# Kernel tuning notes

Hardware: AMD Instinct MI355X
Metric: run time of the kernel (lower is better)

The kernel has to match this reference:

```python
import jax, jax.numpy as jnp
import numpy as np

EDGE_THRESHOLD = 5  # from init_kwargs


def setup_inputs() -> dict:
    key = jax.random.key(0)
    batch = jax.random.normal(key, (2, 512, 192, 256), dtype=jnp.float32)
    return {"batch": batch}


def reference(batch):
    # batch: [b, c, h, w]
    # 1) depth-wise (channel) max
    depth_wise_max = jnp.max(batch, axis=1, keepdims=True)      # [b,1,h,w]
    is_depth_wise_max = batch == depth_wise_max

    # 2) 3x3 local max (stride 1, pad 1) == max_pool2d(3,1,1)
    local_max = jax.lax.reduce_window(
        batch, -jnp.inf, jax.lax.max,
        window_dimensions=(1, 1, 3, 3),
        window_strides=(1, 1, 1, 1),
        padding='SAME')
    is_local_max = batch == local_max

    # 3) fixed 3x3 Hessian stencils via zero-padded shifts (same math as conv2d w/ padding=1)
    z = jnp.pad(batch, ((0, 0), (0, 0), (1, 1), (1, 1)))        # zero pad
    up    = z[:, :, :-2, 1:-1]
    down  = z[:, :, 2:,  1:-1]
    left  = z[:, :, 1:-1, :-2]
    right = z[:, :, 1:-1, 2:]
    dii = up + down - 2.0 * batch                                # [[0,1,0],[0,-2,0],[0,1,0]]
    djj = left + right - 2.0 * batch                             # [[0,0,0],[1,-2,1],[0,0,0]]
    dij = 0.25 * (z[:, :, :-2, :-2] - z[:, :, :-2, 2:]
                  - z[:, :, 2:, :-2] + z[:, :, 2:, 2:])          # 0.25*[[1,0,-1],[0,0,0],[-1,0,1]]

    det = dii * djj - dij * dij
    tr = dii + djj
    threshold = (EDGE_THRESHOLD + 1) ** 2 / EDGE_THRESHOLD
    # torch.min on bool tensors == logical and
    is_not_edge = (tr * tr / det <= threshold) & (det > 0)

    detected = is_depth_wise_max & is_local_max & is_not_edge
    return detected
```

## Files before the change

kernel.cpp:

```cpp
#include <hip/hip_runtime.h>
#include <cstdint>
#include <cstddef>


namespace {

constexpr int Bn = 2;
constexpr int Cn = 512;
constexpr int Hn = 192;
constexpr int Wn = 256;
constexpr int CH  = Hn * Wn;
constexpr int SEG = 8;
constexpr int CPS = Cn / SEG;
constexpr int GPS = CPS / 32;
constexpr int NGROUPS = SEG * GPS;

__global__ __launch_bounds__(512)
void hard_detect_kernel(const float* __restrict__ in, int* __restrict__ out) {
    const int tid = threadIdx.x & 63;
    const int s   = threadIdx.x >> 6;
    const int j   = blockIdx.x * 64 + tid;
    const int i   = blockIdx.y;
    const int b   = blockIdx.z;

    __shared__ uint32_t smask[NGROUPS][64];
    __shared__ float    smaxv[NGROUPS][64];

    const size_t base = ((size_t)b * Cn * Hn + (size_t)i) * Wn + (size_t)j;

    float M = -__builtin_inff();
    for (int g = 0; g < GPS; ++g) {
        uint32_t m = 0u;
        #pragma unroll
        for (int k = 0; k < 32; ++k) {
            const int c = s * CPS + g * 32 + k;
            const size_t idx = base + (size_t)c * (size_t)CH;
            const float v = in[idx];
            __builtin_nontemporal_store(0, &out[idx]);
            if (v > M) { M = v; m = (1u << k); }
            else if (v == M) { m |= (1u << k); }
        }
        smask[s * GPS + g][tid] = m;
        smaxv[s * GPS + g][tid] = M;
    }

    __syncthreads();

    float Mg = smaxv[GPS - 1][tid];
    #pragma unroll
    for (int ss = 1; ss < SEG; ++ss)
        Mg = fmaxf(Mg, smaxv[ss * GPS + GPS - 1][tid]);

    asm volatile("s_waitcnt vmcnt(0)" ::: "memory");

    const bool has_u = (i > 0), has_d = (i < Hn - 1);
    const bool has_l = (j > 0), has_r = (j < Wn - 1);

    for (int g = 0; g < GPS; ++g) {
        if (smaxv[s * GPS + g][tid] != Mg) continue;
        uint32_t m = smask[s * GPS + g][tid];
        while (m) {
            const int k = __ffs(m) - 1;
            m &= (m - 1u);
            const int c = s * CPS + g * 32 + k;
            const size_t p = base + (size_t)c * (size_t)CH;
            const float v = Mg;

            const float nu  = has_u ? in[p - Wn] : 0.0f;
            const float nd  = has_d ? in[p + Wn] : 0.0f;
            const float nl  = has_l ? in[p - 1]  : 0.0f;
            const float nr  = has_r ? in[p + 1]  : 0.0f;
            const float nul = (has_u && has_l) ? in[p - Wn - 1] : 0.0f;
            const float nur = (has_u && has_r) ? in[p - Wn + 1] : 0.0f;
            const float ndl = (has_d && has_l) ? in[p + Wn - 1] : 0.0f;
            const float ndr = (has_d && has_r) ? in[p + Wn + 1] : 0.0f;

            const bool lm =
                (!has_u || v >= nu) && (!has_d || v >= nd) &&
                (!has_l || v >= nl) && (!has_r || v >= nr) &&
                (!(has_u && has_l) || v >= nul) &&
                (!(has_u && has_r) || v >= nur) &&
                (!(has_d && has_l) || v >= ndl) &&
                (!(has_d && has_r) || v >= ndr);

            if (lm) {
                const float dii = (nu + nd) - 2.0f * v;
                const float djj = (nl + nr) - 2.0f * v;
                const float dij = 0.25f * (((nul - nur) - ndl) + ndr);
                const float det = __fmul_rn(dii, djj) - __fmul_rn(dij, dij);
                const float tr  = dii + djj;
                const float ratio = __fmul_rn(tr, tr) / det;
                if (det > 0.0f && ratio <= 7.2f) {
                    out[p] = 1;
                }
            }
        }
    }
}

}

extern "C" void kernel_launch(void* const* d_in, const int* in_sizes, int n_in,
                              void* d_out, int out_size, void* d_ws, size_t ws_size,
                              hipStream_t stream) {
    const float* in = (const float*)d_in[0];
    int* out = (int*)d_out;
    (void)in_sizes; (void)n_in; (void)out_size; (void)d_ws; (void)ws_size;

    dim3 grid(Wn / 64, Hn, Bn);
    dim3 block(512);
    hipLaunchKernelGGL(hard_detect_kernel, grid, block, 0, stream, in, out);
}
```

Before: 68.20 us.

## Vectorize channel-max scan with float4 loads and 16 channel segments per block

Each thread now handles four adjacent columns, using 128-bit loads and 128-bit nontemporal zero stores instead of scalar accesses. The channel dimension is split into 16 segments of 32 channels, so each block has 1024 threads and covers a full row. The grid shrinks to one block per row, which gives 384 blocks in total. The goal is fewer memory instructions and wider transactions on this bandwidth-bound pass, at the cost of less parallelism across blocks and more register pressure.

Measured after the change: 74.09 us. 8.6% more time.

```diff
diff --git a/kernel.cpp b/kernel.cpp
--- a/kernel.cpp
+++ b/kernel.cpp
@@ -10,61 +10,74 @@
 constexpr int Hn = 192;
 constexpr int Wn = 256;
 constexpr int CH  = Hn * Wn;
-constexpr int SEG = 8;
+constexpr int SEG = 16;
 constexpr int CPS = Cn / SEG;
-constexpr int GPS = CPS / 32;
-constexpr int NGROUPS = SEG * GPS;
+constexpr int NGROUPS = SEG;
 
-__global__ __launch_bounds__(512)
+typedef float f32x4 __attribute__((ext_vector_type(4)));
+typedef int   i32x4 __attribute__((ext_vector_type(4)));
+
+__global__ __launch_bounds__(1024)
 void hard_detect_kernel(const float* __restrict__ in, int* __restrict__ out) {
     const int tid = threadIdx.x & 63;
     const int s   = threadIdx.x >> 6;
-    const int j   = blockIdx.x * 64 + tid;
+    const int j0  = tid * 4;
     const int i   = blockIdx.y;
     const int b   = blockIdx.z;
 
-    __shared__ uint32_t smask[NGROUPS][64];
-    __shared__ float    smaxv[NGROUPS][64];
+    __shared__ uint4  smask[NGROUPS][64];
+    __shared__ float4 smaxv[NGROUPS][64];
 
-    const size_t base = ((size_t)b * Cn * Hn + (size_t)i) * Wn + (size_t)j;
+    const size_t base = ((size_t)b * Cn * Hn + (size_t)i) * Wn + (size_t)j0;
 
-    float M = -__builtin_inff();
-    for (int g = 0; g < GPS; ++g) {
-        uint32_t m = 0u;
-        #pragma unroll
-        for (int k = 0; k < 32; ++k) {
-            const int c = s * CPS + g * 32 + k;
-            const size_t idx = base + (size_t)c * (size_t)CH;
-            const float v = in[idx];
-            __builtin_nontemporal_store(0, &out[idx]);
-            if (v > M) { M = v; m = (1u << k); }
-            else if (v == M) { m |= (1u << k); }
-        }
-        smask[s * GPS + g][tid] = m;
-        smaxv[s * GPS + g][tid] = M;
+    float M0 = -__builtin_inff(), M1 = M0, M2 = M0, M3 = M0;
+    uint32_t m0 = 0u, m1 = 0u, m2 = 0u, m3 = 0u;
+    #pragma unroll
+    for (int k = 0; k < CPS; ++k) {
+        const int c = s * CPS + k;
+        const size_t idx = base + (size_t)c * (size_t)CH;
+        const f32x4 v = *reinterpret_cast<const f32x4*>(&in[idx]);
+        const i32x4 z = {0, 0, 0, 0};
+        __builtin_nontemporal_store(z, reinterpret_cast<i32x4*>(&out[idx]));
+        if (v.x > M0) { M0 = v.x; m0 = (1u << k); } else if (v.x == M0) { m0 |= (1u << k); }
+        if (v.y > M1) { M1 = v.y; m1 = (1u << k); } else if (v.y == M1) { m1 |= (1u << k); }
+        if (v.z > M2) { M2 = v.z; m2 = (1u << k); } else if (v.z == M2) { m2 |= (1u << k); }
+        if (v.w > M3) { M3 = v.w; m3 = (1u << k); } else if (v.w == M3) { m3 |= (1u << k); }
     }
+    smask[s][tid] = make_uint4(m0, m1, m2, m3);
+    smaxv[s][tid] = make_float4(M0, M1, M2, M3);
 
     __syncthreads();
 
-    float Mg = smaxv[GPS - 1][tid];
+    float4 Mg = smaxv[0][tid];
     #pragma unroll
-    for (int ss = 1; ss < SEG; ++ss)
-        Mg = fmaxf(Mg, smaxv[ss * GPS + GPS - 1][tid]);
+    for (int ss = 1; ss < SEG; ++ss) {
+        const float4 t = smaxv[ss][tid];
+        Mg.x = fmaxf(Mg.x, t.x);
+        Mg.y = fmaxf(Mg.y, t.y);
+        Mg.z = fmaxf(Mg.z, t.z);
+        Mg.w = fmaxf(Mg.w, t.w);
+    }
 
     asm volatile("s_waitcnt vmcnt(0)" ::: "memory");
 
     const bool has_u = (i > 0), has_d = (i < Hn - 1);
-    const bool has_l = (j > 0), has_r = (j < Wn - 1);
 
-    for (int g = 0; g < GPS; ++g) {
-        if (smaxv[s * GPS + g][tid] != Mg) continue;
-        uint32_t m = smask[s * GPS + g][tid];
+    #pragma unroll
+    for (int col = 0; col < 4; ++col) {
+        const int j = j0 + col;
+        const float Mgc = (col == 0) ? Mg.x : (col == 1) ? Mg.y : (col == 2) ? Mg.z : Mg.w;
+        const float Msc = (col == 0) ? M0   : (col == 1) ? M1   : (col == 2) ? M2   : M3;
+        if (Msc != Mgc) continue;
+        const bool has_l = (j > 0), has_r = (j < Wn - 1);
+
+        uint32_t m = (col == 0) ? m0 : (col == 1) ? m1 : (col == 2) ? m2 : m3;
         while (m) {
             const int k = __ffs(m) - 1;
             m &= (m - 1u);
-            const int c = s * CPS + g * 32 + k;
-            const size_t p = base + (size_t)c * (size_t)CH;
-            const float v = Mg;
+            const int c = s * CPS + k;
+            const size_t p = base + (size_t)col + (size_t)c * (size_t)CH;
+            const float v = Mgc;
 
             const float nu  = has_u ? in[p - Wn] : 0.0f;
             const float nd  = has_d ? in[p + Wn] : 0.0f;
@@ -107,7 +120,7 @@
     int* out = (int*)d_out;
     (void)in_sizes; (void)n_in; (void)out_size; (void)d_ws; (void)ws_size;
 
-    dim3 grid(Wn / 64, Hn, Bn);
-    dim3 block(512);
+    dim3 grid(1, Hn, Bn);
+    dim3 block(1024);
     hipLaunchKernelGGL(hard_detect_kernel, grid, block, 0, stream, in, out);
 }
```

## Two-pass channel max with float2 vectorization, re-reading input instead of masks

Applied to the files above, without the earlier changes.

Replaces the single pass that tracked argmax bitmasks with a plain max reduction over channels using float2 loads and four independent accumulators. A second pass re-reads every input value, compares it to the channel max, and writes both outputs in one 64-bit nontemporal store. Each thread now covers two columns and the grid is halved. This removes the per-element mask bookkeeping and the separate zero-store pass, at the cost of reading the input twice (about 200MB), which may partly hit in cache.

Measured after the change: 106.4 us. +56.1%, slower.

```diff
diff --git a/kernel.cpp b/kernel.cpp
--- a/kernel.cpp
+++ b/kernel.cpp
@@ -12,89 +12,95 @@
 constexpr int CH  = Hn * Wn;
 constexpr int SEG = 8;
 constexpr int CPS = Cn / SEG;
-constexpr int GPS = CPS / 32;
-constexpr int NGROUPS = SEG * GPS;
+
+__device__ __forceinline__ bool eval_candidate(
+    const float* __restrict__ in, size_t p, float v,
+    bool has_u, bool has_d, bool has_l, bool has_r) {
+    const float nu  = has_u ? in[p - Wn] : 0.0f;
+    const float nd  = has_d ? in[p + Wn] : 0.0f;
+    const float nl  = has_l ? in[p - 1]  : 0.0f;
+    const float nr  = has_r ? in[p + 1]  : 0.0f;
+    const float nul = (has_u && has_l) ? in[p - Wn - 1] : 0.0f;
+    const float nur = (has_u && has_r) ? in[p - Wn + 1] : 0.0f;
+    const float ndl = (has_d && has_l) ? in[p + Wn - 1] : 0.0f;
+    const float ndr = (has_d && has_r) ? in[p + Wn + 1] : 0.0f;
+
+    const bool lm =
+        (!has_u || v >= nu) && (!has_d || v >= nd) &&
+        (!has_l || v >= nl) && (!has_r || v >= nr) &&
+        (!(has_u && has_l) || v >= nul) &&
+        (!(has_u && has_r) || v >= nur) &&
+        (!(has_d && has_l) || v >= ndl) &&
+        (!(has_d && has_r) || v >= ndr);
+    if (!lm) return false;
+
+    const float dii = (nu + nd) - 2.0f * v;
+    const float djj = (nl + nr) - 2.0f * v;
+    const float dij = 0.25f * (((nul - nur) - ndl) + ndr);
+    const float det = __fmul_rn(dii, djj) - __fmul_rn(dij, dij);
+    const float tr  = dii + djj;
+    const float ratio = __fmul_rn(tr, tr) / det;
+    return (det > 0.0f) && (ratio <= 7.2f);
+}
 
 __global__ __launch_bounds__(512)
 void hard_detect_kernel(const float* __restrict__ in, int* __restrict__ out) {
     const int tid = threadIdx.x & 63;
     const int s   = threadIdx.x >> 6;
-    const int j   = blockIdx.x * 64 + tid;
+    const int j0  = blockIdx.x * 128 + tid * 2;
     const int i   = blockIdx.y;
     const int b   = blockIdx.z;
 
-    __shared__ uint32_t smask[NGROUPS][64];
-    __shared__ float    smaxv[NGROUPS][64];
+    __shared__ float2 smax[SEG][64];
 
-    const size_t base = ((size_t)b * Cn * Hn + (size_t)i) * Wn + (size_t)j;
+    const size_t base = ((size_t)b * Cn * Hn + (size_t)i) * Wn + (size_t)j0;
+    const size_t seg0 = base + (size_t)(s * CPS) * (size_t)CH;
 
-    float M = -__builtin_inff();
-    for (int g = 0; g < GPS; ++g) {
-        uint32_t m = 0u;
-        #pragma unroll
-        for (int k = 0; k < 32; ++k) {
-            const int c = s * CPS + g * 32 + k;
-            const size_t idx = base + (size_t)c * (size_t)CH;
-            const float v = in[idx];
-            __builtin_nontemporal_store(0, &out[idx]);
-            if (v > M) { M = v; m = (1u << k); }
-            else if (v == M) { m |= (1u << k); }
-        }
-        smask[s * GPS + g][tid] = m;
-        smaxv[s * GPS + g][tid] = M;
+    float a0 = -__builtin_inff(), a1 = a0;
+    float b0 = a0, b1 = a0, c0 = a0, c1 = a0, d0 = a0, d1 = a0;
+    #pragma unroll
+    for (int k = 0; k < CPS; k += 4) {
+        const float2 v0 = *reinterpret_cast<const float2*>(&in[seg0 + (size_t)(k + 0) * CH]);
+        const float2 v1 = *reinterpret_cast<const float2*>(&in[seg0 + (size_t)(k + 1) * CH]);
+        const float2 v2 = *reinterpret_cast<const float2*>(&in[seg0 + (size_t)(k + 2) * CH]);
+        const float2 v3 = *reinterpret_cast<const float2*>(&in[seg0 + (size_t)(k + 3) * CH]);
+        a0 = fmaxf(a0, v0.x); a1 = fmaxf(a1, v0.y);
+        b0 = fmaxf(b0, v1.x); b1 = fmaxf(b1, v1.y);
+        c0 = fmaxf(c0, v2.x); c1 = fmaxf(c1, v2.y);
+        d0 = fmaxf(d0, v3.x); d1 = fmaxf(d1, v3.y);
     }
+    smax[s][tid] = make_float2(fmaxf(fmaxf(a0, b0), fmaxf(c0, d0)),
+                               fmaxf(fmaxf(a1, b1), fmaxf(c1, d1)));
 
     __syncthreads();
 
-    float Mg = smaxv[GPS - 1][tid];
+    float Mg0 = smax[0][tid].x;
+    float Mg1 = smax[0][tid].y;
     #pragma unroll
-    for (int ss = 1; ss < SEG; ++ss)
-        Mg = fmaxf(Mg, smaxv[ss * GPS + GPS - 1][tid]);
+    for (int ss = 1; ss < SEG; ++ss) {
+        Mg0 = fmaxf(Mg0, smax[ss][tid].x);
+        Mg1 = fmaxf(Mg1, smax[ss][tid].y);
+    }
 
-    asm volatile("s_waitcnt vmcnt(0)" ::: "memory");
+    const bool has_u  = (i > 0), has_d = (i < Hn - 1);
+    const bool has_l0 = (j0 > 0);
+    const bool has_r1 = (j0 < Wn - 2);
 
-    const bool has_u = (i > 0), has_d = (i < Hn - 1);
-    const bool has_l = (j > 0), has_r = (j < Wn - 1);
-
-    for (int g = 0; g < GPS; ++g) {
-        if (smaxv[s * GPS + g][tid] != Mg) continue;
-        uint32_t m = smask[s * GPS + g][tid];
-        while (m) {
-            const int k = __ffs(m) - 1;
-            m &= (m - 1u);
-            const int c = s * CPS + g * 32 + k;
-            const size_t p = base + (size_t)c * (size_t)CH;
-            const float v = Mg;
-
-            const float nu  = has_u ? in[p - Wn] : 0.0f;
-            const float nd  = has_d ? in[p + Wn] : 0.0f;
-            const float nl  = has_l ? in[p - 1]  : 0.0f;
-            const float nr  = has_r ? in[p + 1]  : 0.0f;
-            const float nul = (has_u && has_l) ? in[p - Wn - 1] : 0.0f;
-            const float nur = (has_u && has_r) ? in[p - Wn + 1] : 0.0f;
-            const float ndl = (has_d && has_l) ? in[p + Wn - 1] : 0.0f;
-            const float ndr = (has_d && has_r) ? in[p + Wn + 1] : 0.0f;
-
-            const bool lm =
-                (!has_u || v >= nu) && (!has_d || v >= nd) &&
-                (!has_l || v >= nl) && (!has_r || v >= nr) &&
-                (!(has_u && has_l) || v >= nul) &&
-                (!(has_u && has_r) || v >= nur) &&
-                (!(has_d && has_l) || v >= ndl) &&
-                (!(has_d && has_r) || v >= ndr);
-
-            if (lm) {
-                const float dii = (nu + nd) - 2.0f * v;
-                const float djj = (nl + nr) - 2.0f * v;
-                const float dij = 0.25f * (((nul - nur) - ndl) + ndr);
-                const float det = __fmul_rn(dii, djj) - __fmul_rn(dij, dij);
-                const float tr  = dii + djj;
-                const float ratio = __fmul_rn(tr, tr) / det;
-                if (det > 0.0f && ratio <= 7.2f) {
-                    out[p] = 1;
-                }
-            }
+    #pragma unroll 4
+    for (int k = 0; k < CPS; ++k) {
+        const size_t idx = seg0 + (size_t)k * (size_t)CH;
+        const float2 v = *reinterpret_cast<const float2*>(&in[idx]);
+        unsigned long long o = 0ULL;
+        if (v.x == Mg0) {
+            if (eval_candidate(in, idx,     v.x, has_u, has_d, has_l0, true))
+                o |= 1ULL;
         }
+        if (v.y == Mg1) {
+            if (eval_candidate(in, idx + 1, v.y, has_u, has_d, true, has_r1))
+                o |= (1ULL << 32);
+        }
+        __builtin_nontemporal_store(o,
+            reinterpret_cast<unsigned long long*>(&out[idx]));
     }
 }
 
@@ -107,7 +113,7 @@
     int* out = (int*)d_out;
     (void)in_sizes; (void)n_in; (void)out_size; (void)d_ws; (void)ws_size;
 
-    dim3 grid(Wn / 64, Hn, Bn);
+    dim3 grid(Wn / 128, Hn, Bn);
     dim3 block(512);
     hipLaunchKernelGGL(hard_detect_kernel, grid, block, 0, stream, in, out);
 }
```
